# Kernel optimization log

Hardware: AMD Instinct MI355X
Metric: run time of the kernel (lower is better)

Reference implementation:

```python
import jax, jax.numpy as jnp
import numpy as np
from jax import lax

EPS = 1e-10

def _ln(x, g, b):
    m = x.mean(-1, keepdims=True)
    v = x.var(-1, keepdims=True)
    return (x - m) / jnp.sqrt(v + 1e-5) * g + b

def _gather(t, idx):
    # t: (B, HW, c), idx: (B, HW, d) -> (B, HW, d, c); out[n,i,k,:] = t[n, idx[n,i,k], :]
    return jax.vmap(lambda tn, In: tn[In])(t, idx)

def setup_inputs() -> dict:
    key = jax.random.key(0)
    ks = jax.random.split(key, 20)
    b, v, c, d, h, w, hid, ksz = 2, 2, 128, 64, 64, 64, 256, 5
    hw = h * w
    Bf = b * v  # v_1 == 1 target view per reference view
    std = 0.02
    return {
        'features_mv': jax.random.normal(ks[0], (b, v, c, h, w), jnp.float32),
        'warp_indices': jax.random.randint(ks[1], (Bf, hw, d), 0, hw, jnp.int32),
        'depth_prob': jax.random.uniform(ks[2], (Bf, hw, d), jnp.float32),
        'ln1_g': jnp.ones((c,), jnp.float32), 'ln1_b': jnp.zeros((c,), jnp.float32),
        'wq': jax.random.normal(ks[3], (c, c), jnp.float32) * std, 'bq': jnp.zeros((c,), jnp.float32),
        'wk': jax.random.normal(ks[4], (c, c), jnp.float32) * std, 'bk': jnp.zeros((c,), jnp.float32),
        'wv': jax.random.normal(ks[5], (c, c), jnp.float32) * std, 'bv': jnp.zeros((c,), jnp.float32),
        'k_pe': jax.random.normal(ks[6], (1, 1, d), jnp.float32) * std,
        'v_pe': jax.random.normal(ks[7], (1, 1, d), jnp.float32) * std,
        'rpe': jax.random.normal(ks[8], (1, 1, d), jnp.float32) * std,
        'proj_w': jax.random.normal(ks[9], (c, c), jnp.float32) * std, 'proj_b': jnp.zeros((c,), jnp.float32),
        'ln2_g': jnp.ones((c,), jnp.float32), 'ln2_b': jnp.zeros((c,), jnp.float32),
        'fc1_w': jax.random.normal(ks[10], (c, hid), jnp.float32) * std, 'fc1_b': jnp.zeros((hid,), jnp.float32),
        'dw_w': jax.random.normal(ks[11], (hid, 1, ksz, ksz), jnp.float32) * std, 'dw_b': jnp.zeros((hid,), jnp.float32),
        'fc2_w': jax.random.normal(ks[12], (hid, c), jnp.float32) * std, 'fc2_b': jnp.zeros((c,), jnp.float32),
    }

def reference(features_mv, warp_indices, depth_prob, ln1_g, ln1_b, wq, bq, wk, bk, wv, bv,
              k_pe, v_pe, rpe, proj_w, proj_b, ln2_g, ln2_b, fc1_w, fc1_b, dw_w, dw_b, fc2_w, fc2_b):
    b, v, c, h, w = features_mv.shape
    hw = h * w
    hid = fc1_w.shape[1]
    scale = c ** (-0.5)  # num_heads = 1 -> head_dim = dim

    # (b v) (h w) c
    x = features_mv.reshape(b * v, c, hw).transpose(0, 2, 1)
    shortcut = x
    xn = _ln(x, ln1_g, ln1_b)
    q = xn @ wq + bq
    k = xn @ wk + bk
    vv = xn @ wv + bv

    # nn pairing: v=2, v_1=1 -> each reference view attends the other view
    Q = (q.reshape(b, v, hw, c) * scale).reshape(b * v, hw, c)
    K = k.reshape(b, v, hw, c)[:, ::-1].reshape(b * v, hw, c)
    V = vv.reshape(b, v, hw, c)[:, ::-1].reshape(b * v, hw, c)

    # SMM_QmK: cost[n,i,k] = sum_c Q[n,i,c] * K[n, idx[n,i,k], c]
    Kg = _gather(K, warp_indices)                       # (B, hw, d, c)
    cost = jnp.einsum('bic,bikc->bik', Q, Kg)
    Q_pe = Q.sum(-1, keepdims=True)                     # (B, hw, 1)
    cost = cost + Q_pe * k_pe + rpe                     # broadcast (1,1,d)

    # (Sim_UNet similarity refinement omitted: UNetModel source unavailable; identity here)
    attn = jax.nn.softmax(cost, axis=-1)
    attn = attn * depth_prob
    attn = (attn + EPS) / (attn.sum(-1, keepdims=True) + EPS)

    # SMM_AmV: out[n,i,c] = sum_k attn[n,i,k] * V[n, idx[n,i,k], c]
    Vg = _gather(V, warp_indices)                       # (B, hw, d, c)
    out = jnp.einsum('bik,bikc->bic', attn, Vg)
    out = out + (attn * v_pe).sum(-1, keepdims=True)

    # projection + residual (v_1 == 1 so B == b*v)
    x = shortcut + (out @ proj_w + proj_b)

    # ConvFFN residual branch
    xn2 = _ln(x, ln2_g, ln2_b)
    y = jax.nn.gelu(xn2 @ fc1_w + fc1_b, approximate=False)
    yi = y.transpose(0, 2, 1).reshape(b * v, hid, h, w)
    yc = lax.conv_general_dilated(yi, dw_w, (1, 1), 'SAME', feature_group_count=hid,
                                  dimension_numbers=('NCHW', 'OIHW', 'NCHW'))
    yc = jax.nn.gelu(yc + dw_b[None, :, None, None], approximate=False)
    y = y + yc.reshape(b * v, hid, hw).transpose(0, 2, 1)
    y = y @ fc2_w + fc2_b
    return x + y
```

## Files before the change

### kernel.cpp

```cpp
#include <hip/hip_runtime.h>
#include <math.h>

#define TOK   16384
#define HW    4096
#define C     128
#define D     64
#define HID   256

constexpr float LN_EPS = 1e-5f;
constexpr float EPS_R  = 1e-10f;
constexpr float QSCALE = 0.08838834764831845f;

typedef __attribute__((ext_vector_type(8))) short  bf16x8;
typedef __attribute__((ext_vector_type(4))) float  f32x4;
#define MFMA16(a, b, c) __builtin_amdgcn_mfma_f32_16x16x32_bf16((a), (b), (c), 0, 0, 0)

__device__ __forceinline__ float bflo(unsigned u) { return __uint_as_float(u << 16); }
__device__ __forceinline__ float bfhi(unsigned u) { return __uint_as_float(u & 0xffff0000u); }
__device__ __forceinline__ float bfu(unsigned short u) { return __uint_as_float((unsigned)u << 16); }
__device__ __forceinline__ unsigned short f2bf(float f) {
  unsigned u = __float_as_uint(f);
  unsigned r = (u + 0x7fffu + ((u >> 16) & 1u)) >> 16;
  return (unsigned short)r;
}
__device__ __forceinline__ float gelu_exact(float x) {
  return 0.5f * x * (1.0f + erff(x * 0.7071067811865476f));
}

__global__ __launch_bounds__(256) void k_prep(const float* __restrict__ wq,
    const float* __restrict__ wk, const float* __restrict__ wv,
    const float* __restrict__ pw, const float* __restrict__ f1w,
    const float* __restrict__ f2w, unsigned short* __restrict__ wt) {
  int id = blockIdx.x * 256 + threadIdx.x;
  if (id < 16384) {
    int n = id >> 7, k = id & 127;
    wt[id] = f2bf(wq[k * 128 + n]);
  } else if (id < 32768) {
    int e = id - 16384; int n = e >> 7, k = e & 127;
    wt[id] = f2bf(wk[k * 128 + n]);
  } else if (id < 49152) {
    int e = id - 32768; int n = e >> 7, k = e & 127;
    wt[id] = f2bf(wv[k * 128 + n]);
  } else if (id < 65536) {
    int e = id - 49152; int n = e >> 7, k = e & 127;
    wt[id] = f2bf(pw[k * 128 + n]);
  } else if (id < 98304) {
    int e = id - 65536; int n = e >> 7, k = e & 127;
    wt[id] = f2bf(f1w[k * 256 + n]);
  } else if (id < 131072) {
    int e = id - 98304; int n = e >> 8, k = e & 255;
    wt[id] = f2bf(f2w[k * 128 + n]);
  }
}

__global__ __launch_bounds__(256) void k_ln1(const float* __restrict__ feat,
    const float* __restrict__ g, const float* __restrict__ b,
    unsigned short* __restrict__ xnb, float* __restrict__ xtm) {
  __shared__ float tile[64][C + 1];
  int t0 = blockIdx.x * 64;
  int n = t0 / HW, i0 = t0 % HW;
  int tid = threadIdx.x;
  const float* fb = feat + (size_t)n * C * HW;
  for (int e = tid; e < 64 * C; e += 256) {
    int ch = e >> 6, ii = e & 63;
    tile[ii][ch] = fb[(size_t)ch * HW + i0 + ii];
  }
  __syncthreads();
  int wave = tid >> 6, lane = tid & 63;
  for (int tkn = wave; tkn < 64; tkn += 4) {
    float a0 = tile[tkn][lane];
    float a1 = tile[tkn][lane + 64];
    float s = a0 + a1;
    for (int off = 32; off; off >>= 1) s += __shfl_xor(s, off, 64);
    float mean = s * (1.0f / 128.0f);
    float d0 = a0 - mean, d1 = a1 - mean;
    float v = d0 * d0 + d1 * d1;
    for (int off = 32; off; off >>= 1) v += __shfl_xor(v, off, 64);
    float rstd = rsqrtf(v * (1.0f / 128.0f) + LN_EPS);
    size_t ro = (size_t)(t0 + tkn) * C;
    xnb[ro + lane]      = f2bf(d0 * rstd * g[lane] + b[lane]);
    xnb[ro + lane + 64] = f2bf(d1 * rstd * g[lane + 64] + b[lane + 64]);
    xtm[ro + lane]      = a0;
    xtm[ro + lane + 64] = a1;
  }
}

__global__ __launch_bounds__(256) void k_qkv(const unsigned short* __restrict__ xnb,
    const unsigned short* __restrict__ wt,
    const float* __restrict__ bq, const float* __restrict__ bk,
    const float* __restrict__ bv, float* __restrict__ q,
    unsigned short* __restrict__ ksw, unsigned short* __restrict__ vsw) {
  int w = threadIdx.x >> 6, lane = threadIdx.x & 63;
  int q4 = lane >> 4, m = lane & 15;
  int t0 = blockIdx.x * 64 + w * 16;
  int wsel = blockIdx.y;
  const unsigned short* Wt = wt + wsel * 16384;
  const unsigned short* ap = xnb + (size_t)(t0 + m) * C + q4 * 8;
  bf16x8 a[4];
  #pragma unroll
  for (int ks = 0; ks < 4; ks++) a[ks] = *(const bf16x8*)(ap + ks * 32);
  f32x4 acc[8];
  #pragma unroll
  for (int nt = 0; nt < 8; nt++) acc[nt] = (f32x4){0.f, 0.f, 0.f, 0.f};
  #pragma unroll
  for (int nt = 0; nt < 8; nt++) {
    const unsigned short* bp = Wt + (size_t)(nt * 16 + m) * C + q4 * 8;
    #pragma unroll
    for (int ks = 0; ks < 4; ks++) {
      bf16x8 bfrag = *(const bf16x8*)(bp + ks * 32);
      acc[nt] = MFMA16(a[ks], bfrag, acc[nt]);
    }
  }
  if (wsel == 0) {
    #pragma unroll
    for (int nt = 0; nt < 8; nt++) {
      int col = nt * 16 + m;
      float bb = bq[col];
      #pragma unroll
      for (int reg = 0; reg < 4; reg++) {
        int row = t0 + q4 * 4 + reg;
        q[(size_t)row * C + col] = (acc[nt][reg] + bb) * QSCALE;
      }
    }
  } else {
    const float* B = (wsel == 1) ? bk : bv;
    unsigned short* O = (wsel == 1) ? ksw : vsw;
    int n = t0 >> 12, i0 = t0 & 4095;
    int tsw = ((n ^ 1) << 12) + i0;
    #pragma unroll
    for (int nt = 0; nt < 8; nt++) {
      int col = nt * 16 + m;
      float bb = B[col];
      #pragma unroll
      for (int reg = 0; reg < 4; reg++) {
        int row = tsw + q4 * 4 + reg;
        O[(size_t)row * C + col] = f2bf(acc[nt][reg] + bb);
      }
    }
  }
}

__global__ __launch_bounds__(256) void k_attn(const float* __restrict__ q,
    const unsigned short* __restrict__ ksw, const unsigned short* __restrict__ vsw,
    const int* __restrict__ widx, const float* __restrict__ dprob,
    const float* __restrict__ kpe, const float* __restrict__ vpe,
    const float* __restrict__ rpe, unsigned short* __restrict__ aoutb) {
  int lane = threadIdx.x & 63;
  int wave = threadIdx.x >> 6;
  int token = blockIdx.x * 4 + wave;
  int n = token >> 12;
  const unsigned short* Kb = ksw + (size_t)n * HW * C;
  const unsigned short* Vb = vsw + (size_t)n * HW * C;
  int g = lane >> 3, s = lane & 7;
  float qreg[16];
  const float* qp = q + (size_t)token * C + s * 16;
  #pragma unroll
  for (int i = 0; i < 4; i++) {
    float4 t = *(const float4*)(qp + i * 4);
    qreg[i * 4 + 0] = t.x; qreg[i * 4 + 1] = t.y;
    qreg[i * 4 + 2] = t.z; qreg[i * 4 + 3] = t.w;
  }
  float qpe = 0.f;
  #pragma unroll
  for (int i = 0; i < 16; i++) qpe += qreg[i];
  qpe += __shfl_xor(qpe, 1, 64);
  qpe += __shfl_xor(qpe, 2, 64);
  qpe += __shfl_xor(qpe, 4, 64);
  int myidx = widx[token * D + lane];
  float mydp = dprob[token * D + lane];
  float mycost = 0.f;
  #pragma unroll
  for (int pass = 0; pass < 8; ++pass) {
    int row = __shfl(myidx, pass * 8 + g, 64);
    const unsigned short* kr = Kb + (size_t)row * C + s * 16;
    uint4 ka = *(const uint4*)(kr);
    uint4 kb = *(const uint4*)(kr + 8);
    float p;
    p  = bflo(ka.x) * qreg[0]  + bfhi(ka.x) * qreg[1];
    p += bflo(ka.y) * qreg[2]  + bfhi(ka.y) * qreg[3];
    p += bflo(ka.z) * qreg[4]  + bfhi(ka.z) * qreg[5];
    p += bflo(ka.w) * qreg[6]  + bfhi(ka.w) * qreg[7];
    p += bflo(kb.x) * qreg[8]  + bfhi(kb.x) * qreg[9];
    p += bflo(kb.y) * qreg[10] + bfhi(kb.y) * qreg[11];
    p += bflo(kb.z) * qreg[12] + bfhi(kb.z) * qreg[13];
    p += bflo(kb.w) * qreg[14] + bfhi(kb.w) * qreg[15];
    p += __shfl_xor(p, 1, 64);
    p += __shfl_xor(p, 2, 64);
    p += __shfl_xor(p, 4, 64);
    float t = __shfl(p, (lane & 7) << 3, 64);
    if (pass == g) mycost = t;
  }
  mycost += qpe * kpe[lane] + rpe[lane];
  float mx = mycost;
  for (int off = 32; off; off >>= 1) mx = fmaxf(mx, __shfl_xor(mx, off, 64));
  float e = __expf(mycost - mx);
  float ssum = e;
  for (int off = 32; off; off >>= 1) ssum += __shfl_xor(ssum, off, 64);
  float attn = (e / ssum) * mydp;
  float s2 = attn;
  for (int off = 32; off; off >>= 1) s2 += __shfl_xor(s2, off, 64);
  attn = (attn + EPS_R) / (s2 + EPS_R);
  float vpt = attn * vpe[lane];
  for (int off = 32; off; off >>= 1) vpt += __shfl_xor(vpt, off, 64);
  float o0 = vpt, o1 = vpt;
  #pragma unroll 8
  for (int kk = 0; kk < D; ++kk) {
    int row = __shfl(myidx, kk, 64);
    float a = __shfl(attn, kk, 64);
    unsigned v = *(const unsigned*)(Vb + (size_t)row * C + lane * 2);
    o0 += a * bflo(v);
    o1 += a * bfhi(v);
  }
  unsigned pk = (unsigned)f2bf(o0) | ((unsigned)f2bf(o1) << 16);
  *(unsigned*)(aoutb + (size_t)token * C + lane * 2) = pk;
}

__global__ __launch_bounds__(256) void k_projln(const unsigned short* __restrict__ aoutb,
    const unsigned short* __restrict__ wt, const float* __restrict__ pb,
    float* __restrict__ xio, const float* __restrict__ g2,
    const float* __restrict__ b2, unsigned short* __restrict__ xn2b) {
  int w = threadIdx.x >> 6, lane = threadIdx.x & 63;
  int q4 = lane >> 4, m = lane & 15;
  int t0 = blockIdx.x * 64 + w * 16;
  const unsigned short* Wt = wt + 3 * 16384;
  const unsigned short* ap = aoutb + (size_t)(t0 + m) * C + q4 * 8;
  bf16x8 a[4];
  #pragma unroll
  for (int ks = 0; ks < 4; ks++) a[ks] = *(const bf16x8*)(ap + ks * 32);
  f32x4 acc[8];
  #pragma unroll
  for (int nt = 0; nt < 8; nt++) acc[nt] = (f32x4){0.f, 0.f, 0.f, 0.f};
  #pragma unroll
  for (int nt = 0; nt < 8; nt++) {
    const unsigned short* bp = Wt + (size_t)(nt * 16 + m) * C + q4 * 8;
    #pragma unroll
    for (int ks = 0; ks < 4; ks++) {
      bf16x8 bfrag = *(const bf16x8*)(bp + ks * 32);
      acc[nt] = MFMA16(a[ks], bfrag, acc[nt]);
    }
  }
  float s1[4] = {0.f, 0.f, 0.f, 0.f}, s2[4] = {0.f, 0.f, 0.f, 0.f};
  #pragma unroll
  for (int nt = 0; nt < 8; nt++) {
    int col = nt * 16 + m;
    float bb = pb[col];
    #pragma unroll
    for (int reg = 0; reg < 4; reg++) {
      int row = t0 + q4 * 4 + reg;
      float v = acc[nt][reg] + bb + xio[(size_t)row * C + col];
      acc[nt][reg] = v;
      s1[reg] += v;
      s2[reg] += v * v;
    }
  }
  #pragma unroll
  for (int reg = 0; reg < 4; reg++) {
    #pragma unroll
    for (int off = 1; off < 16; off <<= 1) {
      s1[reg] += __shfl_xor(s1[reg], off, 64);
      s2[reg] += __shfl_xor(s2[reg], off, 64);
    }
  }
  float mean[4], rstd[4];
  #pragma unroll
  for (int reg = 0; reg < 4; reg++) {
    mean[reg] = s1[reg] * (1.0f / 128.0f);
    float var = s2[reg] * (1.0f / 128.0f) - mean[reg] * mean[reg];
    rstd[reg] = rsqrtf(var + LN_EPS);
  }
  #pragma unroll
  for (int nt = 0; nt < 8; nt++) {
    int col = nt * 16 + m;
    float gc = g2[col], bc = b2[col];
    #pragma unroll
    for (int reg = 0; reg < 4; reg++) {
      int row = t0 + q4 * 4 + reg;
      float v = acc[nt][reg];
      xio[(size_t)row * C + col] = v;
      xn2b[(size_t)row * C + col] = f2bf((v - mean[reg]) * rstd[reg] * gc + bc);
    }
  }
}

__global__ __launch_bounds__(256) void k_fc1(const unsigned short* __restrict__ xn2b,
    const unsigned short* __restrict__ wt, const float* __restrict__ f1b,
    unsigned short* __restrict__ y) {
  int w = threadIdx.x >> 6, lane = threadIdx.x & 63;
  int q4 = lane >> 4, m = lane & 15;
  int t0 = blockIdx.x * 64 + w * 16;
  int n0 = blockIdx.y * 128;
  const unsigned short* Wt = wt + 65536 + (size_t)n0 * C;
  const unsigned short* ap = xn2b + (size_t)(t0 + m) * C + q4 * 8;
  bf16x8 a[4];
  #pragma unroll
  for (int ks = 0; ks < 4; ks++) a[ks] = *(const bf16x8*)(ap + ks * 32);
  f32x4 acc[8];
  #pragma unroll
  for (int nt = 0; nt < 8; nt++) acc[nt] = (f32x4){0.f, 0.f, 0.f, 0.f};
  #pragma unroll
  for (int nt = 0; nt < 8; nt++) {
    const unsigned short* bp = Wt + (size_t)(nt * 16 + m) * C + q4 * 8;
    #pragma unroll
    for (int ks = 0; ks < 4; ks++) {
      bf16x8 bfrag = *(const bf16x8*)(bp + ks * 32);
      acc[nt] = MFMA16(a[ks], bfrag, acc[nt]);
    }
  }
  #pragma unroll
  for (int nt = 0; nt < 8; nt++) {
    int col = n0 + nt * 16 + m;
    float bb = f1b[col];
    #pragma unroll
    for (int reg = 0; reg < 4; reg++) {
      int row = t0 + q4 * 4 + reg;
      y[(size_t)row * HID + col] = f2bf(gelu_exact(acc[nt][reg] + bb));
    }
  }
}

__global__ __launch_bounds__(256) void k_dwconv(const unsigned short* __restrict__ y,
    const float* __restrict__ w, const float* __restrict__ bias,
    unsigned short* __restrict__ yc) {
  __shared__ float tile[20 * 20][8];
  __shared__ float wl[8][25];
  __shared__ float bl[8];
  int bid = blockIdx.x;
  int tile_id = bid & 15;
  int cb = (bid >> 4) & 31;
  int n = bid >> 9;
  int ty = (tile_id >> 2) * 16, tx = (tile_id & 3) * 16;
  int ch0 = cb * 8;
  int tid = threadIdx.x;
  if (tid < 200) wl[tid / 25][tid % 25] = w[(size_t)(ch0 + tid / 25) * 25 + tid % 25];
  if (tid < 8) bl[tid] = bias[ch0 + tid];
  const unsigned short* yb = y + (size_t)n * HW * HID;
  for (int e = tid; e < 400 * 8; e += 256) {
    int cc = e & 7;
    int p = e >> 3;
    int py = p / 20, px = p % 20;
    int gy = ty + py - 2, gx = tx + px - 2;
    float v = 0.f;
    if (gy >= 0 && gy < 64 && gx >= 0 && gx < 64)
      v = bfu(yb[(size_t)(gy * 64 + gx) * HID + ch0 + cc]);
    tile[p][cc] = v;
  }
  __syncthreads();
  int cc = tid & 7;
  int xx = (tid >> 3) & 15;
  int yg = tid >> 7;
  float wreg[25];
  #pragma unroll
  for (int k = 0; k < 25; k++) wreg[k] = wl[cc][k];
  float bb = bl[cc];
  for (int j = 0; j < 8; ++j) {
    int yy = yg * 8 + j;
    float acc = 0.f;
    #pragma unroll
    for (int dy = 0; dy < 5; ++dy)
      #pragma unroll
      for (int dx = 0; dx < 5; ++dx)
        acc += wreg[dy * 5 + dx] * tile[(yy + dy) * 20 + (xx + dx)][cc];
    acc = gelu_exact(acc + bb);
    yc[(size_t)(n * HW + (ty + yy) * 64 + tx + xx) * HID + ch0 + cc] = f2bf(acc);
  }
}

__global__ __launch_bounds__(256) void k_fc2(const unsigned short* __restrict__ y,
    const unsigned short* __restrict__ ycg, const unsigned short* __restrict__ wt,
    const float* __restrict__ f2b, const float* __restrict__ xio,
    float* __restrict__ outp) {
  int w = threadIdx.x >> 6, lane = threadIdx.x & 63;
  int q4 = lane >> 4, m = lane & 15;
  int t0 = blockIdx.x * 64 + w * 16;
  const unsigned short* Wt = wt + 98304;
  const unsigned short* ap = y + (size_t)(t0 + m) * HID + q4 * 8;
  const unsigned short* cp = ycg + (size_t)(t0 + m) * HID + q4 * 8;
  union U { bf16x8 v; unsigned short s[8]; };
  bf16x8 a[8];
  #pragma unroll
  for (int ks = 0; ks < 8; ks++) {
    U ua, uc, ur;
    ua.v = *(const bf16x8*)(ap + ks * 32);
    uc.v = *(const bf16x8*)(cp + ks * 32);
    #pragma unroll
    for (int j = 0; j < 8; j++) ur.s[j] = f2bf(bfu(ua.s[j]) + bfu(uc.s[j]));
    a[ks] = ur.v;
  }
  f32x4 acc[8];
  #pragma unroll
  for (int nt = 0; nt < 8; nt++) acc[nt] = (f32x4){0.f, 0.f, 0.f, 0.f};
  #pragma unroll
  for (int nt = 0; nt < 8; nt++) {
    const unsigned short* bp = Wt + (size_t)(nt * 16 + m) * HID + q4 * 8;
    #pragma unroll
    for (int ks = 0; ks < 8; ks++) {
      bf16x8 bfrag = *(const bf16x8*)(bp + ks * 32);
      acc[nt] = MFMA16(a[ks], bfrag, acc[nt]);
    }
  }
  #pragma unroll
  for (int nt = 0; nt < 8; nt++) {
    int col = nt * 16 + m;
    float bb = f2b[col];
    #pragma unroll
    for (int reg = 0; reg < 4; reg++) {
      int row = t0 + q4 * 4 + reg;
      outp[(size_t)row * C + col] = acc[nt][reg] + bb + xio[(size_t)row * C + col];
    }
  }
}

extern "C" void kernel_launch(void* const* d_in, const int* in_sizes, int n_in,
                              void* d_out, int out_size, void* d_ws, size_t ws_size,
                              hipStream_t stream) {
  (void)in_sizes; (void)n_in; (void)out_size; (void)ws_size;
  const float* feat  = (const float*)d_in[0];
  const int*   widx  = (const int*)d_in[1];
  const float* dprob = (const float*)d_in[2];
  const float* ln1g  = (const float*)d_in[3];
  const float* ln1b  = (const float*)d_in[4];
  const float* wq    = (const float*)d_in[5];
  const float* bq    = (const float*)d_in[6];
  const float* wk    = (const float*)d_in[7];
  const float* bk    = (const float*)d_in[8];
  const float* wv    = (const float*)d_in[9];
  const float* bv    = (const float*)d_in[10];
  const float* kpe   = (const float*)d_in[11];
  const float* vpe   = (const float*)d_in[12];
  const float* rpe   = (const float*)d_in[13];
  const float* pw    = (const float*)d_in[14];
  const float* pb    = (const float*)d_in[15];
  const float* ln2g  = (const float*)d_in[16];
  const float* ln2b  = (const float*)d_in[17];
  const float* f1w   = (const float*)d_in[18];
  const float* f1b   = (const float*)d_in[19];
  const float* dww   = (const float*)d_in[20];
  const float* dwb   = (const float*)d_in[21];
  const float* f2w   = (const float*)d_in[22];
  const float* f2b   = (const float*)d_in[23];

  float* ws = (float*)d_ws;
  const size_t M2 = (size_t)TOK * C;
  float* qb  = ws;
  float* xio = ws + M2;
  unsigned short* xnb   = (unsigned short*)(ws + 2 * M2);
  unsigned short* ksb   = (unsigned short*)(ws + 2 * M2 + M2 / 2);
  unsigned short* vsb   = (unsigned short*)(ws + 3 * M2);
  unsigned short* aoutb = (unsigned short*)(ws + 3 * M2 + M2 / 2);
  unsigned short* xn2b  = (unsigned short*)(ws + 4 * M2);
  unsigned short* yb    = (unsigned short*)(ws + 4 * M2 + M2 / 2);
  unsigned short* ycgb  = (unsigned short*)(ws + 5 * M2 + M2 / 2);
  unsigned short* wtb   = (unsigned short*)(ws + 6 * M2 + M2 / 2);

  k_prep  <<<512, 256, 0, stream>>>(wq, wk, wv, pw, f1w, f2w, wtb);
  k_ln1   <<<TOK / 64, 256, 0, stream>>>(feat, ln1g, ln1b, xnb, xio);
  k_qkv   <<<dim3(TOK / 64, 3), 256, 0, stream>>>(xnb, wtb, bq, bk, bv, qb, ksb, vsb);
  k_attn  <<<TOK / 4, 256, 0, stream>>>(qb, ksb, vsb, widx, dprob, kpe, vpe, rpe, aoutb);
  k_projln<<<TOK / 64, 256, 0, stream>>>(aoutb, wtb, pb, xio, ln2g, ln2b, xn2b);
  k_fc1   <<<dim3(TOK / 64, 2), 256, 0, stream>>>(xn2b, wtb, f1b, yb);
  k_dwconv<<<2048, 256, 0, stream>>>(yb, dww, dwb, ycgb);
  k_fc2   <<<TOK / 64, 256, 0, stream>>>(yb, ycgb, wtb, f2b, xio, (float*)d_out);
}
```

Baseline: 222.2 us.

## Split GEMM output columns across more blocks, unfuse LN2, remap attention blocks

```diff
diff --git a/kernel.cpp b/kernel.cpp
--- a/kernel.cpp
+++ b/kernel.cpp
@@ -93,18 +93,18 @@
   int w = threadIdx.x >> 6, lane = threadIdx.x & 63;
   int q4 = lane >> 4, m = lane & 15;
   int t0 = blockIdx.x * 64 + w * 16;
-  int wsel = blockIdx.y;
+  int wsel = blockIdx.y >> 1, half = blockIdx.y & 1;
   const unsigned short* Wt = wt + wsel * 16384;
   const unsigned short* ap = xnb + (size_t)(t0 + m) * C + q4 * 8;
   bf16x8 a[4];
   #pragma unroll
   for (int ks = 0; ks < 4; ks++) a[ks] = *(const bf16x8*)(ap + ks * 32);
-  f32x4 acc[8];
-  #pragma unroll
-  for (int nt = 0; nt < 8; nt++) acc[nt] = (f32x4){0.f, 0.f, 0.f, 0.f};
-  #pragma unroll
-  for (int nt = 0; nt < 8; nt++) {
-    const unsigned short* bp = Wt + (size_t)(nt * 16 + m) * C + q4 * 8;
+  f32x4 acc[4];
+  #pragma unroll
+  for (int nt = 0; nt < 4; nt++) acc[nt] = (f32x4){0.f, 0.f, 0.f, 0.f};
+  #pragma unroll
+  for (int nt = 0; nt < 4; nt++) {
+    const unsigned short* bp = Wt + (size_t)(half * 64 + nt * 16 + m) * C + q4 * 8;
     #pragma unroll
     for (int ks = 0; ks < 4; ks++) {
       bf16x8 bfrag = *(const bf16x8*)(bp + ks * 32);
@@ -113,8 +113,8 @@
   }
   if (wsel == 0) {
     #pragma unroll
-    for (int nt = 0; nt < 8; nt++) {
-      int col = nt * 16 + m;
+    for (int nt = 0; nt < 4; nt++) {
+      int col = half * 64 + nt * 16 + m;
       float bb = bq[col];
       #pragma unroll
       for (int reg = 0; reg < 4; reg++) {
@@ -128,8 +128,8 @@
     int n = t0 >> 12, i0 = t0 & 4095;
     int tsw = ((n ^ 1) << 12) + i0;
     #pragma unroll
-    for (int nt = 0; nt < 8; nt++) {
-      int col = nt * 16 + m;
+    for (int nt = 0; nt < 4; nt++) {
+      int col = half * 64 + nt * 16 + m;
       float bb = B[col];
       #pragma unroll
       for (int reg = 0; reg < 4; reg++) {
@@ -147,8 +147,10 @@
     const float* __restrict__ rpe, unsigned short* __restrict__ aoutb) {
   int lane = threadIdx.x & 63;
   int wave = threadIdx.x >> 6;
-  int token = blockIdx.x * 4 + wave;
-  int n = token >> 12;
+  int bid = blockIdx.x;
+  int n = (bid >> 1) & 3;
+  int within = ((bid >> 3) << 1) | (bid & 1);
+  int token = n * HW + within * 4 + wave;
   const unsigned short* Kb = ksw + (size_t)n * HW * C;
   const unsigned short* Vb = vsw + (size_t)n * HW * C;
   int g = lane >> 3, s = lane & 7;
@@ -203,10 +205,11 @@
   float vpt = attn * vpe[lane];
   for (int off = 32; off; off >>= 1) vpt += __shfl_xor(vpt, off, 64);
   float o0 = vpt, o1 = vpt;
-  #pragma unroll 8
+  unsigned att_u = __float_as_uint(attn);
+  #pragma unroll
   for (int kk = 0; kk < D; ++kk) {
-    int row = __shfl(myidx, kk, 64);
-    float a = __shfl(attn, kk, 64);
+    int row = __builtin_amdgcn_readlane(myidx, kk);
+    float a = __uint_as_float(__builtin_amdgcn_readlane(att_u, kk));
     unsigned v = *(const unsigned*)(Vb + (size_t)row * C + lane * 2);
     o0 += a * bflo(v);
     o1 += a * bfhi(v);
@@ -215,70 +218,60 @@
   *(unsigned*)(aoutb + (size_t)token * C + lane * 2) = pk;
 }
 
-__global__ __launch_bounds__(256) void k_projln(const unsigned short* __restrict__ aoutb,
+__global__ __launch_bounds__(256) void k_proj(const unsigned short* __restrict__ aoutb,
     const unsigned short* __restrict__ wt, const float* __restrict__ pb,
-    float* __restrict__ xio, const float* __restrict__ g2,
-    const float* __restrict__ b2, unsigned short* __restrict__ xn2b) {
+    float* xio) {
   int w = threadIdx.x >> 6, lane = threadIdx.x & 63;
   int q4 = lane >> 4, m = lane & 15;
   int t0 = blockIdx.x * 64 + w * 16;
+  int half = blockIdx.y;
   const unsigned short* Wt = wt + 3 * 16384;
   const unsigned short* ap = aoutb + (size_t)(t0 + m) * C + q4 * 8;
   bf16x8 a[4];
   #pragma unroll
   for (int ks = 0; ks < 4; ks++) a[ks] = *(const bf16x8*)(ap + ks * 32);
-  f32x4 acc[8];
-  #pragma unroll
-  for (int nt = 0; nt < 8; nt++) acc[nt] = (f32x4){0.f, 0.f, 0.f, 0.f};
-  #pragma unroll
-  for (int nt = 0; nt < 8; nt++) {
-    const unsigned short* bp = Wt + (size_t)(nt * 16 + m) * C + q4 * 8;
+  f32x4 acc[4];
+  #pragma unroll
+  for (int nt = 0; nt < 4; nt++) acc[nt] = (f32x4){0.f, 0.f, 0.f, 0.f};
+  #pragma unroll
+  for (int nt = 0; nt < 4; nt++) {
+    const unsigned short* bp = Wt + (size_t)(half * 64 + nt * 16 + m) * C + q4 * 8;
     #pragma unroll
     for (int ks = 0; ks < 4; ks++) {
       bf16x8 bfrag = *(const bf16x8*)(bp + ks * 32);
       acc[nt] = MFMA16(a[ks], bfrag, acc[nt]);
     }
   }
-  float s1[4] = {0.f, 0.f, 0.f, 0.f}, s2[4] = {0.f, 0.f, 0.f, 0.f};
-  #pragma unroll
-  for (int nt = 0; nt < 8; nt++) {
-    int col = nt * 16 + m;
+  #pragma unroll
+  for (int nt = 0; nt < 4; nt++) {
+    int col = half * 64 + nt * 16 + m;
     float bb = pb[col];
     #pragma unroll
     for (int reg = 0; reg < 4; reg++) {
       int row = t0 + q4 * 4 + reg;
-      float v = acc[nt][reg] + bb + xio[(size_t)row * C + col];
-      acc[nt][reg] = v;
-      s1[reg] += v;
-      s2[reg] += v * v;
-    }
-  }
-  #pragma unroll
-  for (int reg = 0; reg < 4; reg++) {
-    #pragma unroll
-    for (int off = 1; off < 16; off <<= 1) {
-      s1[reg] += __shfl_xor(s1[reg], off, 64);
-      s2[reg] += __shfl_xor(s2[reg], off, 64);
-    }
-  }
-  float mean[4], rstd[4];
-  #pragma unroll
-  for (int reg = 0; reg < 4; reg++) {
-    mean[reg] = s1[reg] * (1.0f / 128.0f);
-    float var = s2[reg] * (1.0f / 128.0f) - mean[reg] * mean[reg];
-    rstd[reg] = rsqrtf(var + LN_EPS);
-  }
-  #pragma unroll
-  for (int nt = 0; nt < 8; nt++) {
-    int col = nt * 16 + m;
-    float gc = g2[col], bc = b2[col];
-    #pragma unroll
-    for (int reg = 0; reg < 4; reg++) {
-      int row = t0 + q4 * 4 + reg;
-      float v = acc[nt][reg];
-      xio[(size_t)row * C + col] = v;
-      xn2b[(size_t)row * C + col] = f2bf((v - mean[reg]) * rstd[reg] * gc + bc);
-    }
+      size_t ro = (size_t)row * C + col;
+      xio[ro] = acc[nt][reg] + bb + xio[ro];
+    }
+  }
+}
+
+__global__ __launch_bounds__(256) void k_ln2(const float* __restrict__ x,
+    const float* __restrict__ g, const float* __restrict__ b,
+    unsigned short* __restrict__ xn2b) {
+  int wave = threadIdx.x >> 6, lane = threadIdx.x & 63;
+  int tbase = blockIdx.x * 16 + wave * 4;
+  for (int j = 0; j < 4; ++j) {
+    size_t ro = (size_t)(tbase + j) * C;
+    float a0 = x[ro + lane], a1 = x[ro + lane + 64];
+    float s = a0 + a1;
+    for (int off = 32; off; off >>= 1) s += __shfl_xor(s, off, 64);
+    float mean = s * (1.0f / 128.0f);
+    float d0 = a0 - mean, d1 = a1 - mean;
+    float v = d0 * d0 + d1 * d1;
+    for (int off = 32; off; off >>= 1) v += __shfl_xor(v, off, 64);
+    float rstd = rsqrtf(v * (1.0f / 128.0f) + LN_EPS);
+    xn2b[ro + lane]      = f2bf(d0 * rstd * g[lane] + b[lane]);
+    xn2b[ro + lane + 64] = f2bf(d1 * rstd * g[lane + 64] + b[lane + 64]);
   }
 }
 
@@ -288,18 +281,18 @@
   int w = threadIdx.x >> 6, lane = threadIdx.x & 63;
   int q4 = lane >> 4, m = lane & 15;
   int t0 = blockIdx.x * 64 + w * 16;
-  int n0 = blockIdx.y * 128;
-  const unsigned short* Wt = wt + 65536 + (size_t)n0 * C;
+  int cg = blockIdx.y;
+  const unsigned short* Wf = wt + 65536;
   const unsigned short* ap = xn2b + (size_t)(t0 + m) * C + q4 * 8;
   bf16x8 a[4];
   #pragma unroll
   for (int ks = 0; ks < 4; ks++) a[ks] = *(const bf16x8*)(ap + ks * 32);
-  f32x4 acc[8];
-  #pragma unroll
-  for (int nt = 0; nt < 8; nt++) acc[nt] = (f32x4){0.f, 0.f, 0.f, 0.f};
-  #pragma unroll
-  for (int nt = 0; nt < 8; nt++) {
-    const unsigned short* bp = Wt + (size_t)(nt * 16 + m) * C + q4 * 8;
+  f32x4 acc[4];
+  #pragma unroll
+  for (int nt = 0; nt < 4; nt++) acc[nt] = (f32x4){0.f, 0.f, 0.f, 0.f};
+  #pragma unroll
+  for (int nt = 0; nt < 4; nt++) {
+    const unsigned short* bp = Wf + (size_t)(cg * 64 + nt * 16 + m) * C + q4 * 8;
     #pragma unroll
     for (int ks = 0; ks < 4; ks++) {
       bf16x8 bfrag = *(const bf16x8*)(bp + ks * 32);
@@ -307,8 +300,8 @@
     }
   }
   #pragma unroll
-  for (int nt = 0; nt < 8; nt++) {
-    int col = n0 + nt * 16 + m;
+  for (int nt = 0; nt < 4; nt++) {
+    int col = cg * 64 + nt * 16 + m;
     float bb = f1b[col];
     #pragma unroll
     for (int reg = 0; reg < 4; reg++) {
@@ -321,7 +314,7 @@
 __global__ __launch_bounds__(256) void k_dwconv(const unsigned short* __restrict__ y,
     const float* __restrict__ w, const float* __restrict__ bias,
     unsigned short* __restrict__ yc) {
-  __shared__ float tile[20 * 20][8];
+  __shared__ float tile[8][401];
   __shared__ float wl[8][25];
   __shared__ float bl[8];
   int bid = blockIdx.x;
@@ -342,7 +335,7 @@
     float v = 0.f;
     if (gy >= 0 && gy < 64 && gx >= 0 && gx < 64)
       v = bfu(yb[(size_t)(gy * 64 + gx) * HID + ch0 + cc]);
-    tile[p][cc] = v;
+    tile[cc][p] = v;
   }
   __syncthreads();
   int cc = tid & 7;
@@ -359,7 +352,7 @@
     for (int dy = 0; dy < 5; ++dy)
       #pragma unroll
       for (int dx = 0; dx < 5; ++dx)
-        acc += wreg[dy * 5 + dx] * tile[(yy + dy) * 20 + (xx + dx)][cc];
+        acc += wreg[dy * 5 + dx] * tile[cc][(yy + dy) * 20 + (xx + dx)];
     acc = gelu_exact(acc + bb);
     yc[(size_t)(n * HW + (ty + yy) * 64 + tx + xx) * HID + ch0 + cc] = f2bf(acc);
   }
@@ -372,6 +365,7 @@
   int w = threadIdx.x >> 6, lane = threadIdx.x & 63;
   int q4 = lane >> 4, m = lane & 15;
   int t0 = blockIdx.x * 64 + w * 16;
+  int half = blockIdx.y;
   const unsigned short* Wt = wt + 98304;
   const unsigned short* ap = y + (size_t)(t0 + m) * HID + q4 * 8;
   const unsigned short* cp = ycg + (size_t)(t0 + m) * HID + q4 * 8;
@@ -386,12 +380,12 @@
     for (int j = 0; j < 8; j++) ur.s[j] = f2bf(bfu(ua.s[j]) + bfu(uc.s[j]));
     a[ks] = ur.v;
   }
-  f32x4 acc[8];
-  #pragma unroll
-  for (int nt = 0; nt < 8; nt++) acc[nt] = (f32x4){0.f, 0.f, 0.f, 0.f};
-  #pragma unroll
-  for (int nt = 0; nt < 8; nt++) {
-    const unsigned short* bp = Wt + (size_t)(nt * 16 + m) * HID + q4 * 8;
+  f32x4 acc[4];
+  #pragma unroll
+  for (int nt = 0; nt < 4; nt++) acc[nt] = (f32x4){0.f, 0.f, 0.f, 0.f};
+  #pragma unroll
+  for (int nt = 0; nt < 4; nt++) {
+    const unsigned short* bp = Wt + (size_t)(half * 64 + nt * 16 + m) * HID + q4 * 8;
     #pragma unroll
     for (int ks = 0; ks < 8; ks++) {
       bf16x8 bfrag = *(const bf16x8*)(bp + ks * 32);
@@ -399,8 +393,8 @@
     }
   }
   #pragma unroll
-  for (int nt = 0; nt < 8; nt++) {
-    int col = nt * 16 + m;
+  for (int nt = 0; nt < 4; nt++) {
+    int col = half * 64 + nt * 16 + m;
     float bb = f2b[col];
     #pragma unroll
     for (int reg = 0; reg < 4; reg++) {
@@ -454,10 +448,11 @@
 
   k_prep  <<<512, 256, 0, stream>>>(wq, wk, wv, pw, f1w, f2w, wtb);
   k_ln1   <<<TOK / 64, 256, 0, stream>>>(feat, ln1g, ln1b, xnb, xio);
-  k_qkv   <<<dim3(TOK / 64, 3), 256, 0, stream>>>(xnb, wtb, bq, bk, bv, qb, ksb, vsb);
+  k_qkv   <<<dim3(TOK / 64, 6), 256, 0, stream>>>(xnb, wtb, bq, bk, bv, qb, ksb, vsb);
   k_attn  <<<TOK / 4, 256, 0, stream>>>(qb, ksb, vsb, widx, dprob, kpe, vpe, rpe, aoutb);
-  k_projln<<<TOK / 64, 256, 0, stream>>>(aoutb, wtb, pb, xio, ln2g, ln2b, xn2b);
-  k_fc1   <<<dim3(TOK / 64, 2), 256, 0, stream>>>(xn2b, wtb, f1b, yb);
+  k_proj  <<<dim3(TOK / 64, 2), 256, 0, stream>>>(aoutb, wtb, pb, xio);
+  k_ln2   <<<TOK / 16, 256, 0, stream>>>(xio, ln2g, ln2b, xn2b);
+  k_fc1   <<<dim3(TOK / 64, 4), 256, 0, stream>>>(xn2b, wtb, f1b, yb);
   k_dwconv<<<2048, 256, 0, stream>>>(yb, dww, dwb, ycgb);
-  k_fc2   <<<TOK / 64, 256, 0, stream>>>(yb, ycgb, wtb, f2b, xio, (float*)d_out);
-}
+  k_fc2   <<<dim3(TOK / 64, 2), 256, 0, stream>>>(yb, ycgb, wtb, f2b, xio, (float*)d_out);
+}
```

New measurement: 231.3 us. 4.1% more time.
